# Kernel optimization log

Hardware: AMD Instinct MI355X
Metric: run time of the kernel (lower is better)

The kernel has to match this reference:

```python
import jax, jax.numpy as jnp
import numpy as np

BN_EPS = 1e-3  # Keras BatchNormalization default epsilon


def _conv_block(x, k):
    """Per-task conv (stride 2, pad 1) -> ReLU -> BatchNorm (center/scale=False, training).

    x: [B, E, H, W, Cin]  (B tasks, E examples per task)
    k: [B, kh, kw, Cin, Cout]  per-task kernel
    """
    def conv_one(xe, kt):  # xe: [E,H,W,Cin], kt: [kh,kw,Cin,Cout]
        return jax.lax.conv_general_dilated(
            xe, kt, window_strides=(2, 2), padding=[(1, 1), (1, 1)],
            dimension_numbers=('NHWC', 'HWIO', 'NHWC'))
    y = jax.nn.relu(jax.vmap(conv_one)(x, k))  # [B,E,H',W',Cout]
    # BatchNorm in training mode: moments over all axes except channels
    m = jnp.mean(y, axis=(0, 1, 2, 3))
    v = jnp.var(y, axis=(0, 1, 2, 3))
    return (y - m) * jax.lax.rsqrt(v + BN_EPS)


def setup_inputs() -> dict:
    key = jax.random.key(0)
    ks = jax.random.split(key, 6)
    B, E, H, C, O = 64, 64, 28, 64, 20
    return {
        'x': jax.random.normal(ks[0], (B, E, H, H, 1), dtype=jnp.float32),
        'k1': jax.random.normal(ks[1], (B, 3, 3, 1, C), dtype=jnp.float32) * 0.1,
        'k2': jax.random.normal(ks[2], (B, 3, 3, C, C), dtype=jnp.float32) * 0.05,
        'k3': jax.random.normal(ks[3], (B, 3, 3, C, C), dtype=jnp.float32) * 0.05,
        'k4': jax.random.normal(ks[4], (B, 3, 3, C, C), dtype=jnp.float32) * 0.05,
        'w_ro': jax.random.normal(ks[5], (B, C, O), dtype=jnp.float32) * 0.1,
    }


def reference(x, k1, k2, k3, k4, w_ro):
    h = _conv_block(x, k1)   # [B,E,14,14,C]
    h = _conv_block(h, k2)   # [B,E,7,7,C]
    h = _conv_block(h, k3)   # [B,E,4,4,C]
    h = _conv_block(h, k4)   # [B,E,2,2,C]
    # MaxPooling2D with pool size == full spatial extent -> global spatial max
    feat = jnp.max(h, axis=(2, 3))  # [B,E,C]
    # per-task readout matmul: [B,E,H] x [B,H,O] -> [B,E,O]
    return jnp.einsum('beh,bho->beo', feat, w_ro)
```

## Files before the change

kernel.cpp:

```cpp
#include <hip/hip_runtime.h>

#define BN_EPS 1e-3f

typedef __attribute__((ext_vector_type(8))) short bf16x8;
typedef __attribute__((ext_vector_type(16))) float floatx16;
typedef unsigned short u16;

__device__ __forceinline__ u16 f2bf(float f) {
  unsigned u = __float_as_uint(f);
  u += 0x7fffu + ((u >> 16) & 1u);
  return (u16)(u >> 16);
}
__device__ __forceinline__ float bf2f(u16 h) {
  return __uint_as_float(((unsigned)h) << 16);
}

static constexpr int NSHARD = 64;

__global__ __launch_bounds__(256) void c1_k(
    const float* __restrict__ x, const float* __restrict__ k1,
    const float* __restrict__ k3, const float* __restrict__ k4,
    u16* __restrict__ k3T, u16* __restrict__ k4T,
    u16* __restrict__ y1, float* __restrict__ statsSh)
{
  __shared__ __align__(16) char lds[17408];
  const int tid = threadIdx.x;

  if (blockIdx.x >= 4096) {
    float* T = (float*)lds;
    const int blk = blockIdx.x - 4096, l = blk >> 6, b = blk & 63;
    const float* src = (l == 0 ? k3 : k4) + (size_t)b * 9 * 4096;
    u16* dst = (l == 0 ? k3T : k4T) + (size_t)b * 9 * 4096;
    const int cin = tid >> 2, q0 = (tid & 3) * 16;
    const int cout = tid >> 2, ci0 = (tid & 3) * 16;
    for (int s = 0; s < 9; ++s) {
      const float* ss = src + s * 4096;
#pragma unroll
      for (int q = 0; q < 16; q += 4) {
        const float4 v = *(const float4*)(ss + cin * 64 + q0 + q);
        T[(q0 + q + 0) * 68 + cin] = v.x;
        T[(q0 + q + 1) * 68 + cin] = v.y;
        T[(q0 + q + 2) * 68 + cin] = v.z;
        T[(q0 + q + 3) * 68 + cin] = v.w;
      }
      __syncthreads();
      alignas(16) u16 tmp[16];
#pragma unroll
      for (int j = 0; j < 16; ++j) tmp[j] = f2bf(T[cout * 68 + ci0 + j]);
      u16* d = dst + s * 4096 + cout * 64 + ci0;
      *(uint4*)d       = *(uint4*)&tmp[0];
      *(uint4*)(d + 8) = *(uint4*)&tmp[8];
      __syncthreads();
    }
    return;
  }

  float* xp     = (float*)lds;
  float* w1s    = (float*)(lds + 4320);
  float* redsum = (float*)(lds + 6624);
  float* redss  = (float*)(lds + 6880);

  const int be = blockIdx.x, b = be >> 6;
  const int lane = tid & 63, wave = tid >> 6;
  const int l31 = lane & 31, kq8 = (lane >> 5) * 8;

  for (int i = tid; i < 1080; i += 256) xp[i] = 0.f;
  for (int i = tid; i < 576; i += 256) w1s[i] = k1[(size_t)b * 576 + i];
  if (tid < 64) { redsum[tid] = 0.f; redss[tid] = 0.f; }
  __syncthreads();
  for (int i = tid; i < 784; i += 256) {
    const int r = i / 28, c = i - 28 * r;
    xp[(r + 1) * 36 + (c + 1)] = x[(size_t)be * 784 + i];
  }
  __syncthreads();

  bf16x8 bf0, bf1;
#pragma unroll
  for (int j = 0; j < 8; ++j) {
    const int k = kq8 + j;
    bf0[j] = (k < 9) ? (short)f2bf(w1s[k * 64 + l31]) : (short)0;
    bf1[j] = (k < 9) ? (short)f2bf(w1s[k * 64 + 32 + l31]) : (short)0;
  }

  float s0 = 0.f, q0v = 0.f, s1v = 0.f, q1v = 0.f;
  for (int t = wave; t < 7; t += 4) {
    const int row = t * 32 + l31;
    const int p = row < 196 ? row : 195;
    const int oy = p / 14, ox = p - 14 * oy;
    bf16x8 af;
#pragma unroll
    for (int j = 0; j < 8; ++j) {
      const int k = kq8 + j;
      float v = 0.f;
      if (k < 9) v = xp[(2 * oy + k / 3) * 36 + (2 * ox + k % 3)];
      af[j] = (short)f2bf(v);
    }
    floatx16 z;
#pragma unroll
    for (int r = 0; r < 16; ++r) z[r] = 0.f;
    floatx16 c0 = __builtin_amdgcn_mfma_f32_32x32x16_bf16(af, bf0, z, 0, 0, 0);
    floatx16 c1 = __builtin_amdgcn_mfma_f32_32x32x16_bf16(af, bf1, z, 0, 0, 0);
    const int rb = t * 32 + 4 * (lane >> 5);
#pragma unroll
    for (int r = 0; r < 16; ++r) {
      const int rw = rb + (r & 3) + 8 * (r >> 2);
      if (rw < 196) {
        const float v0 = fmaxf(c0[r], 0.f), v1 = fmaxf(c1[r], 0.f);
        const size_t ob = ((size_t)be * 196 + rw) * 64;
        y1[ob + l31]      = f2bf(v0);
        y1[ob + 32 + l31] = f2bf(v1);
        s0 += v0;  q0v = fmaf(v0, v0, q0v);
        s1v += v1; q1v = fmaf(v1, v1, q1v);
      }
    }
  }
  atomicAdd(&redsum[l31], s0);
  atomicAdd(&redss[l31], q0v);
  atomicAdd(&redsum[32 + l31], s1v);
  atomicAdd(&redss[32 + l31], q1v);
  __syncthreads();
  if (tid < 64) {
    const int sh = be & (NSHARD - 1);
    atomicAdd(&statsSh[sh * 128 + tid], redsum[tid]);
    atomicAdd(&statsSh[sh * 128 + 64 + tid], redss[tid]);
  }
}

__global__ __launch_bounds__(256) void foldw_k(
    const float* __restrict__ W, const float* __restrict__ statsSh, float invN,
    u16* __restrict__ Wf, float* __restrict__ biasCls)
{
  __shared__ float T[64 * 68];
  __shared__ float P[256];
  __shared__ float s1[64], t1[64];
  __shared__ float tbS[64];

  const int b = blockIdx.x / 3, sg = blockIdx.x % 3;
  const int tid = threadIdx.x;

  {
    const int g = tid >> 7, cidx = tid & 127;
    float acc = 0.f;
    for (int k = 0; k < NSHARD / 2; ++k)
      acc += statsSh[(g * (NSHARD / 2) + k) * 128 + cidx];
    P[tid] = acc;
  }
  __syncthreads();
  if (tid < 64) {
    const float m = (P[tid] + P[tid + 128]) * invN;
    const float var = fmaf(-m, m, (P[64 + tid] + P[192 + tid]) * invN);
    const float s = rsqrtf(var + BN_EPS);
    s1[tid] = s;
    t1[tid] = -m * s;
  }
  __syncthreads();

  const int cin = tid >> 2, q0 = (tid & 3) * 16;
  const int cout = tid >> 2, ci0 = (tid & 3) * 16;
  for (int s = sg * 3; s < sg * 3 + 3; ++s) {
    if (tid < 64) tbS[tid] = 0.f;
    const float* ss = W + ((size_t)b * 9 + s) * 4096;
#pragma unroll
    for (int q = 0; q < 16; q += 4) {
      const float4 v = *(const float4*)(ss + cin * 64 + q0 + q);
      T[(q0 + q + 0) * 68 + cin] = v.x;
      T[(q0 + q + 1) * 68 + cin] = v.y;
      T[(q0 + q + 2) * 68 + cin] = v.z;
      T[(q0 + q + 3) * 68 + cin] = v.w;
    }
    __syncthreads();
    alignas(16) u16 tmp[16];
    float tb = 0.f;
#pragma unroll
    for (int j = 0; j < 16; ++j) {
      const float wv = T[cout * 68 + ci0 + j];
      tmp[j] = f2bf(wv * s1[ci0 + j]);
      tb = fmaf(t1[ci0 + j], wv, tb);
    }
    u16* dst = Wf + ((size_t)b * 9 + s) * 4096 + cout * 64 + ci0;
    *(uint4*)dst       = *(uint4*)&tmp[0];
    *(uint4*)(dst + 8) = *(uint4*)&tmp[8];
    atomicAdd(&tbS[cout], tb);
    __syncthreads();
    if (tid < 64) {
      const int ky = s / 3, kx = s % 3;
      const float tv = tbS[tid];
#pragma unroll
      for (int cls = 0; cls < 9; ++cls) {
        const int ry = cls / 3, rx = cls % 3;
        const bool valid = !((ry == 1 && ky == 0) || (ry == 2 && ky == 2) ||
                             (rx == 1 && kx == 0) || (rx == 2 && kx == 2));
        if (valid) atomicAdd(&biasCls[(size_t)b * 576 + cls * 64 + tid], tv);
      }
    }
    __syncthreads();
  }
}

__global__ __launch_bounds__(256) void cg2_k(
    const u16* __restrict__ y1, const u16* __restrict__ k2f,
    const float* __restrict__ biasCls, u16* __restrict__ y2,
    float* __restrict__ statsSh)
{
  __shared__ __align__(16) u16 AS[256 * 72];
  __shared__ __align__(16) u16 BtS[64 * 72];
  __shared__ float biasS[576];
  __shared__ float redsum[64], redss[64];

  const int b = blockIdx.x >> 4, e0 = (blockIdx.x & 15) * 4;
  const int tid = threadIdx.x, lane = tid & 63, wave = tid >> 6;
  const int l31 = lane & 31, kq8 = (lane >> 5) * 8;

  for (int i = tid; i < 576; i += 256) biasS[i] = biasCls[(size_t)b * 576 + i];
  if (tid < 64) { redsum[tid] = 0.f; redss[tid] = 0.f; }
  for (int i = tid; i < 480; i += 256) {
    const int row = 196 + (i >> 3), c8 = (i & 7) * 8;
    *(uint4*)&AS[row * 72 + c8] = uint4{0, 0, 0, 0};
  }

  const size_t yb = (size_t)(b * 64 + e0) * 196 * 64;
  const u16* wb = k2f + (size_t)b * 9 * 4096;
  const int bco = tid >> 2, bci = (tid & 3) * 16;
  const int m0 = wave * 64;

  floatx16 acc00, acc01, acc10, acc11;
#pragma unroll
  for (int r = 0; r < 16; ++r) {
    acc00[r] = 0.f; acc01[r] = 0.f; acc10[r] = 0.f; acc11[r] = 0.f;
  }

  for (int s = 0; s < 9; ++s) {
    const int ky = s / 3, kx = s % 3;
    for (int i = tid; i < 1568; i += 256) {
      const int row = i >> 3, c8 = (i & 7) * 8;
      const int e_l = row / 49, pp = row % 49;
      const int oy = pp / 7, ox = pp % 7;
      const int iy = 2 * oy - 1 + ky, ix = 2 * ox - 1 + kx;
      uint4 v = uint4{0, 0, 0, 0};
      if ((unsigned)iy < 14u && (unsigned)ix < 14u)
        v = *(const uint4*)(y1 + yb + ((size_t)e_l * 196 + iy * 14 + ix) * 64 + c8);
      *(uint4*)&AS[row * 72 + c8] = v;
    }
    {
      const u16* g = wb + s * 4096 + bco * 64 + bci;
      *(uint4*)&BtS[bco * 72 + bci]     = *(const uint4*)g;
      *(uint4*)&BtS[bco * 72 + bci + 8] = *(const uint4*)(g + 8);
    }
    __syncthreads();
#pragma unroll
    for (int kk = 0; kk < 4; ++kk) {
      const int ko = kk * 16 + kq8;
      bf16x8 a0 = *(const bf16x8*)&AS[(m0 + l31) * 72 + ko];
      bf16x8 a1 = *(const bf16x8*)&AS[(m0 + 32 + l31) * 72 + ko];
      bf16x8 b0 = *(const bf16x8*)&BtS[l31 * 72 + ko];
      bf16x8 b1 = *(const bf16x8*)&BtS[(32 + l31) * 72 + ko];
      acc00 = __builtin_amdgcn_mfma_f32_32x32x16_bf16(a0, b0, acc00, 0, 0, 0);
      acc01 = __builtin_amdgcn_mfma_f32_32x32x16_bf16(a0, b1, acc01, 0, 0, 0);
      acc10 = __builtin_amdgcn_mfma_f32_32x32x16_bf16(a1, b0, acc10, 0, 0, 0);
      acc11 = __builtin_amdgcn_mfma_f32_32x32x16_bf16(a1, b1, acc11, 0, 0, 0);
    }
    __syncthreads();
  }

  float ls0 = 0.f, lss0 = 0.f, ls1 = 0.f, lss1 = 0.f;
  const int col0 = l31, col1 = 32 + l31;
#pragma unroll
  for (int mt = 0; mt < 2; ++mt) {
    const floatx16& aN0 = mt ? acc10 : acc00;
    const floatx16& aN1 = mt ? acc11 : acc01;
    const int rbb = m0 + mt * 32 + 4 * (lane >> 5);
#pragma unroll
    for (int r = 0; r < 16; ++r) {
      const int rw = rbb + (r & 3) + 8 * (r >> 2);
      if (rw < 196) {
        const int e_l = rw / 49, pr = rw % 49;
        const int ooy = pr / 7, oox = pr % 7;
        const int ry = (ooy == 0) ? 1 : 0;
        const int rx = (oox == 0) ? 1 : 0;
        const int cls = ry * 3 + rx;
        const size_t ob = ((size_t)(b * 64 + e0 + e_l) * 49 + pr) * 64;
        const float v0 = fmaxf(aN0[r] + biasS[cls * 64 + col0], 0.f);
        const float v1 = fmaxf(aN1[r] + biasS[cls * 64 + col1], 0.f);
        y2[ob + col0] = f2bf(v0);
        y2[ob + col1] = f2bf(v1);
        ls0 += v0; lss0 = fmaf(v0, v0, lss0);
        ls1 += v1; lss1 = fmaf(v1, v1, lss1);
      }
    }
  }
  atomicAdd(&redsum[col0], ls0);
  atomicAdd(&redss[col0], lss0);
  atomicAdd(&redsum[col1], ls1);
  atomicAdd(&redss[col1], lss1);
  __syncthreads();
  if (tid < 64) {
    const int sh = blockIdx.x & (NSHARD - 1);
    atomicAdd(&statsSh[sh * 128 + tid], redsum[tid]);
    atomicAdd(&statsSh[sh * 128 + 64 + tid], redss[tid]);
  }
}

template <int Hin, int Hout, int G>
__device__ __forceinline__ void conv_core_bn(
    const u16* __restrict__ yin, const u16* __restrict__ wT,
    const float* __restrict__ statsPrev, float invN, u16* __restrict__ yout,
    float* __restrict__ statsSh, int blk)
{
  constexpr int PPI  = Hout * Hout;
  constexpr int ROWS = G * PPI;
  constexpr int BPT  = 64 / G;
  constexpr int MR   = G * Hin * Hin;
  constexpr int ZR   = MR;

  __shared__ __align__(16) u16 mapS[(MR + 1) * 72];
  __shared__ float P[256];
  __shared__ float s1[64], t1[64];
  __shared__ float redsum[64], redss[64];

  const int b = blk / BPT, e0 = (blk % BPT) * G;
  const int tid = threadIdx.x, lane = tid & 63, wave = tid >> 6;

  if (tid < 64) { redsum[tid] = 0.f; redss[tid] = 0.f; }
  if (tid < 9) *(uint4*)&mapS[ZR * 72 + tid * 8] = uint4{0, 0, 0, 0};
  {
    const int cidx = tid & 127, g = tid >> 7;
    float a = 0.f;
    for (int k = 0; k < NSHARD / 2; ++k)
      a += statsPrev[(g * (NSHARD / 2) + k) * 128 + cidx];
    P[tid] = a;
  }
  __syncthreads();
  if (tid < 64) {
    const float m = (P[tid] + P[tid + 128]) * invN;
    const float var = fmaf(-m, m, (P[64 + tid] + P[192 + tid]) * invN);
    const float s = rsqrtf(var + BN_EPS);
    s1[tid] = s;
    t1[tid] = -m * s;
  }
  __syncthreads();

  {
    const u16* src = yin + (size_t)(b * 64 + e0) * (Hin * Hin) * 64;
    for (int ch = tid; ch < MR * 8; ch += 256) {
      const int r = ch >> 3, c0 = (ch & 7) * 8;
      uint4 v = *(const uint4*)(src + ch * 8);
      const u16* h = (const u16*)&v;
      alignas(16) u16 o[8];
#pragma unroll
      for (int j = 0; j < 8; ++j)
        o[j] = f2bf(fmaf(bf2f(h[j]), s1[c0 + j], t1[c0 + j]));
      *(uint4*)&mapS[r * 72 + c0] = *(uint4*)o;
    }
  }

  const int m0 = (wave & 1) * 32, n0 = (wave >> 1) * 32;
  const int l31 = lane & 31, kq8 = (lane >> 5) * 8;
  const int lrow = m0 + l31;
  const bool rv = lrow < ROWS;
  const int img = rv ? lrow / PPI : 0;
  const int pp  = rv ? lrow % PPI : 0;
  const int oy = pp / Hout, ox = pp % Hout;
  const u16* wbB = wT + (size_t)b * 9 * 4096 + (n0 + l31) * 64 + kq8;

  floatx16 acc;
#pragma unroll
  for (int r = 0; r < 16; ++r) acc[r] = 0.f;

  __syncthreads();

#pragma unroll
  for (int s = 0; s < 9; ++s) {
    const int ky = s / 3, kx = s % 3;
    int pix = ZR;
    if (rv) {
      const int iy = 2 * oy - 1 + ky, ix = 2 * ox - 1 + kx;
      if ((unsigned)iy < (unsigned)Hin && (unsigned)ix < (unsigned)Hin)
        pix = img * (Hin * Hin) + iy * Hin + ix;
    }
    const u16* ap = &mapS[pix * 72 + kq8];
    const u16* bp = wbB + s * 4096;
#pragma unroll
    for (int kk = 0; kk < 4; ++kk) {
      bf16x8 a  = *(const bf16x8*)(ap + kk * 16);
      bf16x8 bv = *(const bf16x8*)(bp + kk * 16);
      acc = __builtin_amdgcn_mfma_f32_32x32x16_bf16(a, bv, acc, 0, 0, 0);
    }
  }

  const int col = n0 + l31;
  const int rb = m0 + 4 * (lane >> 5);
  float ls = 0.f, lss = 0.f;
#pragma unroll
  for (int r = 0; r < 16; ++r) {
    const int rw = rb + (r & 3) + 8 * (r >> 2);
    if (rw < ROWS) {
      const int re = rw / PPI, pr = rw % PPI;
      const float v = fmaxf(acc[r], 0.f);
      yout[((size_t)(b * 64 + e0 + re) * PPI + pr) * 64 + col] = f2bf(v);
      ls += v;
      lss = fmaf(v, v, lss);
    }
  }
  atomicAdd(&redsum[col], ls);
  atomicAdd(&redss[col], lss);
  __syncthreads();
  if (tid < 64) {
    const int sh = blk & (NSHARD - 1);
    atomicAdd(&statsSh[sh * 128 + tid], redsum[tid]);
    atomicAdd(&statsSh[sh * 128 + 64 + tid], redss[tid]);
  }
}

__global__ __launch_bounds__(256) void cg3_k(
    const u16* __restrict__ yin, const u16* __restrict__ wT,
    const float* __restrict__ stPrev, float invN, u16* __restrict__ yout,
    float* __restrict__ statsSh) {
  conv_core_bn<7, 4, 4>(yin, wT, stPrev, invN, yout, statsSh, blockIdx.x);
}
__global__ __launch_bounds__(256) void cg4_k(
    const u16* __restrict__ yin, const u16* __restrict__ wT,
    const float* __restrict__ stPrev, float invN, u16* __restrict__ yout,
    float* __restrict__ statsSh) {
  conv_core_bn<4, 2, 16>(yin, wT, stPrev, invN, yout, statsSh, blockIdx.x);
}

__global__ __launch_bounds__(256) void readout_k(
    const u16* __restrict__ y4, const float* __restrict__ w_ro,
    const float* __restrict__ statsSh, float invN, float* __restrict__ outp)
{
  __shared__ float wl[64 * 20];
  __shared__ float feat[64 * 64];
  __shared__ float P[256];
  __shared__ float sArr[64], tArr[64];

  const int b = blockIdx.x, tid = threadIdx.x;

  {
    const int g = tid >> 7, cidx = tid & 127;
    float acc = 0.f;
    for (int k = 0; k < NSHARD / 2; ++k)
      acc += statsSh[(g * (NSHARD / 2) + k) * 128 + cidx];
    P[tid] = acc;
  }
  for (int i = tid; i < 1280; i += 256) wl[i] = w_ro[(size_t)b * 1280 + i];
  __syncthreads();
  if (tid < 64) {
    const float m = (P[tid] + P[tid + 128]) * invN;
    const float var = fmaf(-m, m, (P[64 + tid] + P[192 + tid]) * invN);
    const float s = rsqrtf(var + BN_EPS);
    sArr[tid] = s;
    tArr[tid] = -m * s;
  }
  __syncthreads();

  {
    const int e = tid & 63;
    for (int c = tid >> 6; c < 64; c += 4) {
      const u16* p4 = y4 + ((size_t)(b * 64 + e) * 4) * 64 + c;
      const float v = fmaxf(fmaxf(bf2f(p4[0]), bf2f(p4[64])),
                            fmaxf(bf2f(p4[128]), bf2f(p4[192])));
      feat[c * 64 + e] = fmaf(v, sArr[c], tArr[c]);
    }
  }
  __syncthreads();

  const int e = tid >> 2, og = (tid & 3) * 5;
  float acc[5] = {0.f, 0.f, 0.f, 0.f, 0.f};
  for (int c = 0; c < 64; ++c) {
    const float f = feat[c * 64 + e];
#pragma unroll
    for (int j = 0; j < 5; ++j) acc[j] = fmaf(f, wl[c * 20 + og + j], acc[j]);
  }
#pragma unroll
  for (int j = 0; j < 5; ++j)
    outp[((size_t)b * 64 + e) * 20 + og + j] = acc[j];
}

extern "C" void kernel_launch(void* const* d_in, const int* in_sizes, int n_in,
                              void* d_out, int out_size, void* d_ws, size_t ws_size,
                              hipStream_t stream) {
  (void)in_sizes; (void)n_in; (void)out_size; (void)ws_size;
  const float* x   = (const float*)d_in[0];
  const float* k1  = (const float*)d_in[1];
  const float* k2  = (const float*)d_in[2];
  const float* k3  = (const float*)d_in[3];
  const float* k4  = (const float*)d_in[4];
  const float* wro = (const float*)d_in[5];
  float* out = (float*)d_out;
  char* ws = (char*)d_ws;

  float* stats = (float*)ws;
  float* bias2 = (float*)(ws + 131072);
  u16* k2f = (u16*)(ws + 278528);
  u16* k3T = (u16*)(ws + 4997120);
  u16* k4T = (u16*)(ws + 9715712);
  u16* y2  = (u16*)(ws + 14434304);
  u16* y1  = (u16*)(ws + 40124416);
  u16* y3  = y1;
  u16* y4  = y3 + (size_t)4194304;

  float* st1 = stats;
  float* st2 = stats + 8192;
  float* st3 = stats + 16384;
  float* st4 = stats + 24576;

  hipMemsetAsync(stats, 0, 131072 + 147456, stream);

  c1_k<<<4224, 256, 0, stream>>>(x, k1, k3, k4, k3T, k4T, y1, st1);
  foldw_k<<<192, 256, 0, stream>>>(k2, st1, 1.f / 802816.f, k2f, bias2);
  cg2_k<<<1024, 256, 0, stream>>>(y1, k2f, bias2, y2, st2);
  cg3_k<<<1024, 256, 0, stream>>>(y2, k3T, st2, 1.f / 200704.f, y3, st3);
  cg4_k<<<256, 256, 0, stream>>>(y3, k4T, st3, 1.f / 65536.f, y4, st4);
  readout_k<<<64, 256, 0, stream>>>(y4, wro, st4, 1.f / 16384.f, out);
}
```

Baseline: 268.7 us.

## Restructure conv2 as one-example blocks with an LDS-resident input map and direct weight loads

The conv2 kernel now gives one example to each block (4096 blocks instead of 1024). It stages the whole 14x14x64 input map in LDS once instead of re-gathering an im2col tile per filter tap. Each wave computes a 32x32 output tile, indexing the map directly per tap and pointing padded positions at a zero row. Weights are read straight from global or cache instead of being staged in LDS. This removes eight of the nine gather passes and the per-tap barriers, but adds more blocks, waste on the 49-row M dimension padded to 64, and uncached-LDS weight fetches.

```diff
diff --git a/kernel.cpp b/kernel.cpp
--- a/kernel.cpp
+++ b/kernel.cpp
@@ -202,99 +202,77 @@
     const float* __restrict__ biasCls, u16* __restrict__ y2,
     float* __restrict__ statsSh)
 {
-  __shared__ __align__(16) u16 AS[256 * 72];
-  __shared__ __align__(16) u16 BtS[64 * 72];
+  __shared__ __align__(16) u16 mapS[197 * 72];
   __shared__ float biasS[576];
   __shared__ float redsum[64], redss[64];
 
-  const int b = blockIdx.x >> 4, e0 = (blockIdx.x & 15) * 4;
-  const int tid = threadIdx.x, lane = tid & 63, wave = tid >> 6;
+  const int be = blockIdx.x, b = be >> 6, tid = threadIdx.x;
+  const int lane = tid & 63, wave = tid >> 6;
   const int l31 = lane & 31, kq8 = (lane >> 5) * 8;
 
   for (int i = tid; i < 576; i += 256) biasS[i] = biasCls[(size_t)b * 576 + i];
   if (tid < 64) { redsum[tid] = 0.f; redss[tid] = 0.f; }
-  for (int i = tid; i < 480; i += 256) {
-    const int row = 196 + (i >> 3), c8 = (i & 7) * 8;
-    *(uint4*)&AS[row * 72 + c8] = uint4{0, 0, 0, 0};
-  }
-
-  const size_t yb = (size_t)(b * 64 + e0) * 196 * 64;
-  const u16* wb = k2f + (size_t)b * 9 * 4096;
-  const int bco = tid >> 2, bci = (tid & 3) * 16;
-  const int m0 = wave * 64;
-
-  floatx16 acc00, acc01, acc10, acc11;
-#pragma unroll
-  for (int r = 0; r < 16; ++r) {
-    acc00[r] = 0.f; acc01[r] = 0.f; acc10[r] = 0.f; acc11[r] = 0.f;
-  }
-
+  if (tid < 9) *(uint4*)&mapS[196 * 72 + tid * 8] = uint4{0, 0, 0, 0};
+
+  {
+    const u16* src = y1 + (size_t)be * 196 * 64;
+    for (int ch = tid; ch < 1568; ch += 256) {
+      const int r = ch >> 3, c8 = (ch & 7) * 8;
+      *(uint4*)&mapS[r * 72 + c8] = *(const uint4*)(src + ch * 8);
+    }
+  }
+
+  const int m0 = (wave & 1) * 32, n0 = (wave >> 1) * 32;
+  const int lrow = m0 + l31;
+  const bool rv = lrow < 49;
+  const int oy = rv ? lrow / 7 : 0, ox = rv ? lrow % 7 : 0;
+  const u16* wbB = k2f + (size_t)b * 9 * 4096 + (n0 + l31) * 64 + kq8;
+
+  floatx16 acc;
+#pragma unroll
+  for (int r = 0; r < 16; ++r) acc[r] = 0.f;
+
+  __syncthreads();
+
+#pragma unroll
   for (int s = 0; s < 9; ++s) {
     const int ky = s / 3, kx = s % 3;
-    for (int i = tid; i < 1568; i += 256) {
-      const int row = i >> 3, c8 = (i & 7) * 8;
-      const int e_l = row / 49, pp = row % 49;
-      const int oy = pp / 7, ox = pp % 7;
+    int pix = 196;
+    if (rv) {
       const int iy = 2 * oy - 1 + ky, ix = 2 * ox - 1 + kx;
-      uint4 v = uint4{0, 0, 0, 0};
-      if ((unsigned)iy < 14u && (unsigned)ix < 14u)
-        v = *(const uint4*)(y1 + yb + ((size_t)e_l * 196 + iy * 14 + ix) * 64 + c8);
-      *(uint4*)&AS[row * 72 + c8] = v;
-    }
-    {
-      const u16* g = wb + s * 4096 + bco * 64 + bci;
-      *(uint4*)&BtS[bco * 72 + bci]     = *(const uint4*)g;
-      *(uint4*)&BtS[bco * 72 + bci + 8] = *(const uint4*)(g + 8);
-    }
-    __syncthreads();
+      if ((unsigned)iy < 14u && (unsigned)ix < 14u) pix = iy * 14 + ix;
+    }
+    const u16* ap = &mapS[pix * 72 + kq8];
+    const u16* bp = wbB + s * 4096;
 #pragma unroll
     for (int kk = 0; kk < 4; ++kk) {
-      const int ko = kk * 16 + kq8;
-      bf16x8 a0 = *(const bf16x8*)&AS[(m0 + l31) * 72 + ko];
-      bf16x8 a1 = *(const bf16x8*)&AS[(m0 + 32 + l31) * 72 + ko];
-      bf16x8 b0 = *(const bf16x8*)&BtS[l31 * 72 + ko];
-      bf16x8 b1 = *(const bf16x8*)&BtS[(32 + l31) * 72 + ko];
-      acc00 = __builtin_amdgcn_mfma_f32_32x32x16_bf16(a0, b0, acc00, 0, 0, 0);
-      acc01 = __builtin_amdgcn_mfma_f32_32x32x16_bf16(a0, b1, acc01, 0, 0, 0);
-      acc10 = __builtin_amdgcn_mfma_f32_32x32x16_bf16(a1, b0, acc10, 0, 0, 0);
-      acc11 = __builtin_amdgcn_mfma_f32_32x32x16_bf16(a1, b1, acc11, 0, 0, 0);
-    }
-    __syncthreads();
-  }
-
-  float ls0 = 0.f, lss0 = 0.f, ls1 = 0.f, lss1 = 0.f;
-  const int col0 = l31, col1 = 32 + l31;
-#pragma unroll
-  for (int mt = 0; mt < 2; ++mt) {
-    const floatx16& aN0 = mt ? acc10 : acc00;
-    const floatx16& aN1 = mt ? acc11 : acc01;
-    const int rbb = m0 + mt * 32 + 4 * (lane >> 5);
-#pragma unroll
-    for (int r = 0; r < 16; ++r) {
-      const int rw = rbb + (r & 3) + 8 * (r >> 2);
-      if (rw < 196) {
-        const int e_l = rw / 49, pr = rw % 49;
-        const int ooy = pr / 7, oox = pr % 7;
-        const int ry = (ooy == 0) ? 1 : 0;
-        const int rx = (oox == 0) ? 1 : 0;
-        const int cls = ry * 3 + rx;
-        const size_t ob = ((size_t)(b * 64 + e0 + e_l) * 49 + pr) * 64;
-        const float v0 = fmaxf(aN0[r] + biasS[cls * 64 + col0], 0.f);
-        const float v1 = fmaxf(aN1[r] + biasS[cls * 64 + col1], 0.f);
-        y2[ob + col0] = f2bf(v0);
-        y2[ob + col1] = f2bf(v1);
-        ls0 += v0; lss0 = fmaf(v0, v0, lss0);
-        ls1 += v1; lss1 = fmaf(v1, v1, lss1);
-      }
-    }
-  }
-  atomicAdd(&redsum[col0], ls0);
-  atomicAdd(&redss[col0], lss0);
-  atomicAdd(&redsum[col1], ls1);
-  atomicAdd(&redss[col1], lss1);
-  __syncthreads();
-  if (tid < 64) {
-    const int sh = blockIdx.x & (NSHARD - 1);
+      bf16x8 a  = *(const bf16x8*)(ap + kk * 16);
+      bf16x8 bv = *(const bf16x8*)(bp + kk * 16);
+      acc = __builtin_amdgcn_mfma_f32_32x32x16_bf16(a, bv, acc, 0, 0, 0);
+    }
+  }
+
+  const int col = n0 + l31;
+  const int rb = m0 + 4 * (lane >> 5);
+  float ls = 0.f, lss = 0.f;
+#pragma unroll
+  for (int r = 0; r < 16; ++r) {
+    const int rw = rb + (r & 3) + 8 * (r >> 2);
+    if (rw < 49) {
+      const int ooy = rw / 7, oox = rw % 7;
+      const int ry = (ooy == 0) ? 1 : 0;
+      const int rx = (oox == 0) ? 1 : 0;
+      const float v = fmaxf(acc[r] + biasS[(ry * 3 + rx) * 64 + col], 0.f);
+      y2[((size_t)be * 49 + rw) * 64 + col] = f2bf(v);
+      ls += v;
+      lss = fmaf(v, v, lss);
+    }
+  }
+  atomicAdd(&redsum[col], ls);
+  atomicAdd(&redss[col], lss);
+  __syncthreads();
+  if (tid < 64) {
+    const int sh = be & (NSHARD - 1);
     atomicAdd(&statsSh[sh * 128 + tid], redsum[tid]);
     atomicAdd(&statsSh[sh * 128 + 64 + tid], redss[tid]);
   }
@@ -508,7 +486,7 @@
 
   c1_k<<<4224, 256, 0, stream>>>(x, k1, k3, k4, k3T, k4T, y1, st1);
   foldw_k<<<192, 256, 0, stream>>>(k2, st1, 1.f / 802816.f, k2f, bias2);
-  cg2_k<<<1024, 256, 0, stream>>>(y1, k2f, bias2, y2, st2);
+  cg2_k<<<4096, 256, 0, stream>>>(y1, k2f, bias2, y2, st2);
   cg3_k<<<1024, 256, 0, stream>>>(y2, k3T, st2, 1.f / 200704.f, y3, st3);
   cg4_k<<<256, 256, 0, stream>>>(y3, k4T, st3, 1.f / 65536.f, y4, st4);
   readout_k<<<64, 256, 0, stream>>>(y4, wro, st4, 1.f / 16384.f, out);
```

New measurement: 276.8 us. 1.03x slower.
